# Optimization experiments

Hardware: AMD Instinct MI355X
Metric: run time of the kernel (lower is better)

## Reference

```python
import jax, jax.numpy as jnp
import numpy as np

SEQ, BATCH, D = 256, 4096, 100  # D = 2*hidden_size
STD = 0.05


def setup_inputs() -> dict:
    key = jax.random.key(0)
    k1, k2, k3, k4, k5 = jax.random.split(key, 5)
    return {
        "f_output": jax.random.normal(k1, (SEQ, BATCH, D), dtype=jnp.float32),
        "h_output": jax.random.normal(k2, (2, BATCH, D // 2), dtype=jnp.float32),
        "sentence_weight": jax.random.normal(k3, (D, D), dtype=jnp.float32) * STD,
        "sentence_bias": jax.random.normal(k4, (1, D), dtype=jnp.float32) * STD,
        "context_weight": jax.random.normal(k5, (D, 1), dtype=jnp.float32) * STD,
    }


def reference(f_output, h_output, sentence_weight, sentence_bias, context_weight):
    # matrix_mul: per-timestep mm + bias + tanh, vectorized over seq. [S,B,D]
    u = jnp.tanh(jnp.einsum('sbd,de->sbe', f_output, sentence_weight) + sentence_bias)
    # context projection (matrix_mul with no bias still applies tanh), squeeze -> [S,B]
    scores = jnp.tanh(jnp.einsum('sbd,dk->sbk', u, context_weight))[..., 0]
    # F.softmax on [B,S] defaults to dim=1 => softmax over seq
    attn = jax.nn.softmax(scores, axis=0)  # [S,B]
    # element_wise_mul: weighted sum over seq, keepdim -> [1,B,D]
    pooled = jnp.sum(f_output * attn[:, :, None], axis=0, keepdims=True)
    return (pooled, h_output)
```

## Files before the change

### kernel.cpp

```cpp
#include <hip/hip_runtime.h>
#include <hip/hip_bf16.h>

#define SEQ 256
#define BATCH 4096
#define DD 100
#define SB (BATCH * DD)
#define NBCOL 8
#define SCH 8
#define NCHUNK (SEQ / SCH)
#define ROWS (SCH * NBCOL)
#define SLAB_B (NBCOL * DD * 4)
#define WROWS_B (16 * DD * 4)

typedef __attribute__((ext_vector_type(8))) short bf16x8;
typedef __attribute__((ext_vector_type(4))) float f32x4;
typedef __attribute__((ext_vector_type(4))) unsigned u32x4;

#define WAIT_VM7  asm volatile("s_waitcnt vmcnt(7)" ::: "memory")
#define WAIT_VM0  asm volatile("s_waitcnt vmcnt(0)" ::: "memory")
#define WAIT_LGKM asm volatile("s_waitcnt lgkmcnt(0)" ::: "memory")

__device__ __forceinline__ short f2bf(float x) {
    __hip_bfloat16 hv = __float2bfloat16(x);
    return *reinterpret_cast<short*>(&hv);
}
__device__ __forceinline__ float bf2f_lo(unsigned int u) {
    return __builtin_bit_cast(float, u << 16);
}
__device__ __forceinline__ float bf2f_hi(unsigned int u) {
    return __builtin_bit_cast(float, u & 0xffff0000u);
}
__device__ __forceinline__ float fast_tanh(float x) {
    float ax = fabsf(x);
    float e  = __expf(-2.0f * ax);
    float t  = (1.0f - e) * __builtin_amdgcn_rcpf(1.0f + e);
    return copysignf(t, x);
}
__device__ __forceinline__ float pade_tanh(float x) {
    const float x2  = x * x;
    const float num = x * (27.0f + x2);
    const float den = fmaf(9.0f, x2, 27.0f);
    const float t   = num * __builtin_amdgcn_rcpf(den);
    return fminf(1.0f, fmaxf(-1.0f, t));
}
__device__ __forceinline__ unsigned pack_bf2(float lo, float hi) {
    return __builtin_amdgcn_perm(__builtin_bit_cast(unsigned, hi),
                                 __builtin_bit_cast(unsigned, lo),
                                 0x07060302u);
}

__global__ void prep_wfrag(const float* __restrict__ W, uint4* __restrict__ wsf) {
    const int idx = blockIdx.x * 256 + threadIdx.x;
    if (idx >= 28 * 64) return;
    const int l  = idx & 63;
    const int ft = idx >> 6;
    const int t  = ft & 3;
    const int n  = ft >> 2;
    const int col   = 16 * n + (l & 15);
    const int kbase = 32 * t + 8 * (l >> 4);
    unsigned short v[8];
    #pragma unroll
    for (int e = 0; e < 8; ++e) {
        const int k = kbase + e;
        const float w = (col < DD && k < DD) ? W[k * DD + col] : 0.0f;
        v[e] = (unsigned short)f2bf(w);
    }
    uint4 u;
    u.x = (unsigned)v[0] | ((unsigned)v[1] << 16);
    u.y = (unsigned)v[2] | ((unsigned)v[3] << 16);
    u.z = (unsigned)v[4] | ((unsigned)v[5] << 16);
    u.w = (unsigned)v[6] | ((unsigned)v[7] << 16);
    wsf[ft * 64 + l] = u;
}

__device__ __forceinline__ void stage_rows(const float* __restrict__ f,
                                           int s0, int b0, float* lbase,
                                           int wid, int lane) {
    const int base = WROWS_B * wid;
    #pragma unroll
    for (int r = 0; r < 6; ++r) {
        const int L   = base + (r << 10) + (lane << 4);
        const int s   = L / SLAB_B;
        const int rem = L - s * SLAB_B;
        const float* gp = f + (size_t)(s0 + s) * SB + (size_t)b0 * DD + (rem >> 2);
        __builtin_amdgcn_global_load_lds(
            (const __attribute__((address_space(1))) void*)gp,
            (__attribute__((address_space(3))) void*)((char*)lbase + L),
            16, 0, 0);
    }
    {
        const int L   = base + 6144 + (lane << 2);
        const int s   = L / SLAB_B;
        const int rem = L - s * SLAB_B;
        const float* gp = f + (size_t)(s0 + s) * SB + (size_t)b0 * DD + (rem >> 2);
        __builtin_amdgcn_global_load_lds(
            (const __attribute__((address_space(1))) void*)gp,
            (__attribute__((address_space(3))) void*)((char*)lbase + L),
            4, 0, 0);
    }
}

__global__ __launch_bounds__(256, 2)
void fused_sent_attn(const float* __restrict__ f,
                     const uint4* __restrict__ wsf,
                     const float* __restrict__ bias,
                     const float* __restrict__ cw,
                     const float* __restrict__ h,
                     float* __restrict__ out)
{
    __shared__ __align__(16) float fs[3][ROWS * DD];
    __shared__ uint4 wlds3[7 * 16];

    const int tid  = threadIdx.x;
    const int lane = tid & 63;
    const int wid  = tid >> 6;
    const int lr   = lane & 15;
    const int g    = lane >> 4;
    const int b0   = blockIdx.x * NBCOL;

    if (tid < 7 * 16) wlds3[tid] = wsf[(4 * (tid >> 4) + 3) * 64 + (tid & 15)];

    float bias_r[7], cw_r[7];
    #pragma unroll
    for (int n = 0; n < 7; ++n) {
        const int c = 16 * n + lr;
        bias_r[n] = (c < DD) ? bias[c] : 0.0f;
        cw_r[n]   = (c < DD) ? cw[c]   : 0.0f;
    }
    {
        const size_t obase = (size_t)BATCH * DD;
        const size_t HB = (size_t)BATCH * 50;
        if (tid < 200) {
            const int half = tid / 100, rem = tid - 100 * half;
            const float4* hs = reinterpret_cast<const float4*>(h + half * HB + (size_t)b0 * 50);
            float4* od = reinterpret_cast<float4*>(out + obase + half * HB + (size_t)b0 * 50);
            od[rem] = hs[rem];
        }
    }
    bf16x8 wr[21];
    #pragma unroll
    for (int n = 0; n < 7; ++n)
        #pragma unroll
        for (int t = 0; t < 3; ++t)
            wr[3 * n + t] = *reinterpret_cast<const bf16x8*>(&wsf[(4 * n + t) * 64 + lane]);
    WAIT_VM0;

    stage_rows(f, 0,   b0, fs[0], wid, lane);
    stage_rows(f, SCH, b0, fs[1], wid, lane);
    WAIT_VM7;
    WAIT_LGKM;
    __builtin_amdgcn_s_barrier();
    __builtin_amdgcn_sched_barrier(0);

    float pacc[4][8] = {{0}};
    float dreg = 0.0f;

    int cur = 0;
    for (int jc = 0; jc < NCHUNK; ++jc) {
        const int nxt2 = (cur + 2 >= 3) ? cur - 1 : cur + 2;

        if (jc + 2 < NCHUNK)
            stage_rows(f, (jc + 2) * SCH, b0, fs[nxt2], wid, lane);

        const float* rp = &fs[cur][(16 * wid + lr) * DD];
        bf16x8 a[4];
        #pragma unroll
        for (int t = 0; t < 3; ++t) {
            const float4 u0 = *reinterpret_cast<const float4*>(rp + 32 * t + 8 * g);
            const float4 u1 = *reinterpret_cast<const float4*>(rp + 32 * t + 8 * g + 4);
            u32x4 pk = {pack_bf2(u0.x, u0.y), pack_bf2(u0.z, u0.w),
                        pack_bf2(u1.x, u1.y), pack_bf2(u1.z, u1.w)};
            a[t] = __builtin_bit_cast(bf16x8, pk);
        }
        {
            u32x4 pk = {0u, 0u, 0u, 0u};
            if (g == 0) {
                const float4 u0 = *reinterpret_cast<const float4*>(rp + 96);
                pk.x = pack_bf2(u0.x, u0.y);
                pk.y = pack_bf2(u0.z, u0.w);
            }
            a[3] = __builtin_bit_cast(bf16x8, pk);
        }

        float scp[4] = {0, 0, 0, 0};
        #pragma unroll
        for (int n = 0; n < 7; ++n) {
            bf16x8 b3 = {0, 0, 0, 0, 0, 0, 0, 0};
            if (g == 0) b3 = *reinterpret_cast<const bf16x8*>(&wlds3[16 * n + lr]);
            f32x4 acc = {bias_r[n], bias_r[n], bias_r[n], bias_r[n]};
            acc = __builtin_amdgcn_mfma_f32_16x16x32_bf16(a[0], wr[3 * n + 0], acc, 0, 0, 0);
            acc = __builtin_amdgcn_mfma_f32_16x16x32_bf16(a[1], wr[3 * n + 1], acc, 0, 0, 0);
            acc = __builtin_amdgcn_mfma_f32_16x16x32_bf16(a[2], wr[3 * n + 2], acc, 0, 0, 0);
            acc = __builtin_amdgcn_mfma_f32_16x16x32_bf16(a[3], b3,            acc, 0, 0, 0);
            #pragma unroll
            for (int r = 0; r < 4; ++r)
                scp[r] = fmaf(pade_tanh(acc[r]), cw_r[n], scp[r]);
        }
        #pragma unroll
        for (int r = 0; r < 4; ++r) {
            float v = scp[r];
            v += __shfl_xor(v, 1);
            v += __shfl_xor(v, 2);
            v += __shfl_xor(v, 4);
            v += __shfl_xor(v, 8);
            scp[r] = v;
        }
        {
            const int src = (lr >> 2) << 4;
            const float tt0 = __shfl(scp[0], src);
            const float tt1 = __shfl(scp[1], src);
            const float tt2 = __shfl(scp[2], src);
            const float tt3 = __shfl(scp[3], src);
            const float ta = (lr & 1) ? tt1 : tt0;
            const float tb = (lr & 1) ? tt3 : tt2;
            const float Srow = (lr & 2) ? tb : ta;
            const float w = __expf(fast_tanh(Srow));

            #pragma unroll
            for (int t = 0; t < 4; ++t) {
                const u32x4 u = __builtin_bit_cast(u32x4, a[t]);
                #pragma unroll
                for (int j = 0; j < 4; ++j) {
                    pacc[t][2 * j]     = fmaf(w, bf2f_lo(u[j]), pacc[t][2 * j]);
                    pacc[t][2 * j + 1] = fmaf(w, bf2f_hi(u[j]), pacc[t][2 * j + 1]);
                }
            }
            dreg += w;
        }

        if (jc + 2 < NCHUNK) { WAIT_VM7; } else { WAIT_VM0; }
        __builtin_amdgcn_sched_barrier(0);
        cur = (cur + 1 >= 3) ? 0 : cur + 1;
    }

    float pv[4][8];
    #pragma unroll
    for (int t = 0; t < 4; ++t)
        #pragma unroll
        for (int e = 0; e < 8; ++e)
            pv[t][e] = pacc[t][e] + __shfl_xor(pacc[t][e], 8);
    const float dv = dreg + __shfl_xor(dreg, 8);

    __syncthreads();

    float* pool_sc = &fs[0][0];
    float* den_sc  = &fs[1][0];
    if (lr < 8) {
        float* dst = pool_sc + (wid * 8 + lr) * 104;
        #pragma unroll
        for (int t = 0; t < 3; ++t) {
            const int d0 = 32 * t + 8 * g;
            const float4 v0 = {pv[t][0], pv[t][1], pv[t][2], pv[t][3]};
            const float4 v1 = {pv[t][4], pv[t][5], pv[t][6], pv[t][7]};
            *reinterpret_cast<float4*>(dst + d0)     = v0;
            *reinterpret_cast<float4*>(dst + d0 + 4) = v1;
        }
        if (g == 0) {
            const float4 v0 = {pv[3][0], pv[3][1], pv[3][2], pv[3][3]};
            *reinterpret_cast<float4*>(dst + 96) = v0;
            den_sc[wid * 8 + lr] = dv;
        }
    }
    __syncthreads();

    if (tid < 200) {
        const int pb = tid / 25, q4 = tid % 25;
        f32x4 acc = {0.0f, 0.0f, 0.0f, 0.0f};
        float den = 0.0f;
        #pragma unroll
        for (int w2 = 0; w2 < 4; ++w2) {
            const f32x4 v = *reinterpret_cast<const f32x4*>(
                pool_sc + (w2 * 8 + pb) * 104 + 4 * q4);
            acc.x += v.x; acc.y += v.y; acc.z += v.z; acc.w += v.w;
            den += den_sc[w2 * 8 + pb];
        }
        const float rd = 1.0f / den;
        float4 o;
        o.x = acc.x * rd; o.y = acc.y * rd; o.z = acc.z * rd; o.w = acc.w * rd;
        *reinterpret_cast<float4*>(&out[(size_t)(b0 + pb) * DD + 4 * q4]) = o;
    }
}

extern "C" void kernel_launch(void* const* d_in, const int* in_sizes, int n_in,
                              void* d_out, int out_size, void* d_ws, size_t ws_size,
                              hipStream_t stream) {
    const float* f    = (const float*)d_in[0];
    const float* h    = (const float*)d_in[1];
    const float* W    = (const float*)d_in[2];
    const float* bias = (const float*)d_in[3];
    const float* cw   = (const float*)d_in[4];
    float* out = (float*)d_out;

    uint4* wsf = (uint4*)d_ws;

    prep_wfrag<<<7, 256, 0, stream>>>(W, wsf);
    fused_sent_attn<<<BATCH / NBCOL, 256, 0, stream>>>(f, wsf, bias, cw, h, out);
}
```

Baseline: 96.84 us.

## Split sequence across two block groups with partial sums and a combine kernel

Each block now covers 16 batch columns and half of the sequence, so every wave stages one contiguous per-timestep plane instead of 8x8 mixed rows. Each block writes unnormalized numerators and denominators to workspace, and a new combine kernel adds the two halves and divides. The grid size stays the same while the staging addressing gets simpler and the cross-lane shuffle reduction goes away. In exchange it adds an extra kernel launch and a round trip of partial results through global memory. The softmax skips max subtraction, which is valid because tanh bounds the scores.

```diff
diff --git a/kernel.cpp b/kernel.cpp
--- a/kernel.cpp
+++ b/kernel.cpp
@@ -5,12 +5,15 @@
 #define BATCH 4096
 #define DD 100
 #define SB (BATCH * DD)
-#define NBCOL 8
-#define SCH 8
-#define NCHUNK (SEQ / SCH)
+#define NBCOL 16
+#define SCH 4
+#define NSGRP 2
+#define SHALF (SEQ / NSGRP)
+#define NCHUNK (SHALF / SCH)
+#define NCGRP (BATCH / NBCOL)
 #define ROWS (SCH * NBCOL)
-#define SLAB_B (NBCOL * DD * 4)
-#define WROWS_B (16 * DD * 4)
+#define PLANE_B (NBCOL * DD * 4)
+#define PSTRIDE 1664
 
 typedef __attribute__((ext_vector_type(8))) short bf16x8;
 typedef __attribute__((ext_vector_type(4))) float f32x4;
@@ -73,40 +76,36 @@
     wsf[ft * 64 + l] = u;
 }
 
-__device__ __forceinline__ void stage_rows(const float* __restrict__ f,
-                                           int s0, int b0, float* lbase,
-                                           int wid, int lane) {
-    const int base = WROWS_B * wid;
+__device__ __forceinline__ void stage_plane(const float* __restrict__ f,
+                                            int s, int b0, float* lbase,
+                                            int wid, int lane) {
+    const int base = PLANE_B * wid;
+    const char* gp0 = (const char*)(f + (size_t)s * SB + (size_t)b0 * DD);
     #pragma unroll
     for (int r = 0; r < 6; ++r) {
-        const int L   = base + (r << 10) + (lane << 4);
-        const int s   = L / SLAB_B;
-        const int rem = L - s * SLAB_B;
-        const float* gp = f + (size_t)(s0 + s) * SB + (size_t)b0 * DD + (rem >> 2);
+        const int off = (r << 10) + (lane << 4);
         __builtin_amdgcn_global_load_lds(
-            (const __attribute__((address_space(1))) void*)gp,
-            (__attribute__((address_space(3))) void*)((char*)lbase + L),
+            (const __attribute__((address_space(1))) void*)(gp0 + off),
+            (__attribute__((address_space(3))) void*)((char*)lbase + base + off),
             16, 0, 0);
     }
     {
-        const int L   = base + 6144 + (lane << 2);
-        const int s   = L / SLAB_B;
-        const int rem = L - s * SLAB_B;
-        const float* gp = f + (size_t)(s0 + s) * SB + (size_t)b0 * DD + (rem >> 2);
+        const int off = 6144 + (lane << 2);
         __builtin_amdgcn_global_load_lds(
-            (const __attribute__((address_space(1))) void*)gp,
-            (__attribute__((address_space(3))) void*)((char*)lbase + L),
+            (const __attribute__((address_space(1))) void*)(gp0 + off),
+            (__attribute__((address_space(3))) void*)((char*)lbase + base + off),
             4, 0, 0);
     }
 }
 
 __global__ __launch_bounds__(256, 2)
-void fused_sent_attn(const float* __restrict__ f,
-                     const uint4* __restrict__ wsf,
-                     const float* __restrict__ bias,
-                     const float* __restrict__ cw,
-                     const float* __restrict__ h,
-                     float* __restrict__ out)
+void part_attn(const float* __restrict__ f,
+               const uint4* __restrict__ wsf,
+               const float* __restrict__ bias,
+               const float* __restrict__ cw,
+               const float* __restrict__ h,
+               float* __restrict__ out,
+               float* __restrict__ part)
 {
     __shared__ __align__(16) float fs[3][ROWS * DD];
     __shared__ uint4 wlds3[7 * 16];
@@ -116,7 +115,11 @@
     const int wid  = tid >> 6;
     const int lr   = lane & 15;
     const int g    = lane >> 4;
-    const int b0   = blockIdx.x * NBCOL;
+    const int bid  = blockIdx.x;
+    const int sgrp = bid >> 8;
+    const int cgrp = bid & (NCGRP - 1);
+    const int b0   = cgrp * NBCOL;
+    const int s_base = sgrp * SHALF;
 
     if (tid < 7 * 16) wlds3[tid] = wsf[(4 * (tid >> 4) + 3) * 64 + (tid & 15)];
 
@@ -127,11 +130,11 @@
         bias_r[n] = (c < DD) ? bias[c] : 0.0f;
         cw_r[n]   = (c < DD) ? cw[c]   : 0.0f;
     }
-    {
+    if (sgrp == 0) {
         const size_t obase = (size_t)BATCH * DD;
         const size_t HB = (size_t)BATCH * 50;
-        if (tid < 200) {
-            const int half = tid / 100, rem = tid - 100 * half;
+        for (int i = tid; i < 400; i += 256) {
+            const int half = i / 200, rem = i - 200 * half;
             const float4* hs = reinterpret_cast<const float4*>(h + half * HB + (size_t)b0 * 50);
             float4* od = reinterpret_cast<float4*>(out + obase + half * HB + (size_t)b0 * 50);
             od[rem] = hs[rem];
@@ -145,8 +148,8 @@
             wr[3 * n + t] = *reinterpret_cast<const bf16x8*>(&wsf[(4 * n + t) * 64 + lane]);
     WAIT_VM0;
 
-    stage_rows(f, 0,   b0, fs[0], wid, lane);
-    stage_rows(f, SCH, b0, fs[1], wid, lane);
+    stage_plane(f, s_base + wid,       b0, fs[0], wid, lane);
+    stage_plane(f, s_base + SCH + wid, b0, fs[1], wid, lane);
     WAIT_VM7;
     WAIT_LGKM;
     __builtin_amdgcn_s_barrier();
@@ -160,7 +163,7 @@
         const int nxt2 = (cur + 2 >= 3) ? cur - 1 : cur + 2;
 
         if (jc + 2 < NCHUNK)
-            stage_rows(f, (jc + 2) * SCH, b0, fs[nxt2], wid, lane);
+            stage_plane(f, s_base + (jc + 2) * SCH + wid, b0, fs[nxt2], wid, lane);
 
         const float* rp = &fs[cur][(16 * wid + lr) * DD];
         bf16x8 a[4];
@@ -233,52 +236,57 @@
         cur = (cur + 1 >= 3) ? 0 : cur + 1;
     }
 
-    float pv[4][8];
-    #pragma unroll
-    for (int t = 0; t < 4; ++t)
-        #pragma unroll
-        for (int e = 0; e < 8; ++e)
-            pv[t][e] = pacc[t][e] + __shfl_xor(pacc[t][e], 8);
-    const float dv = dreg + __shfl_xor(dreg, 8);
-
     __syncthreads();
 
     float* pool_sc = &fs[0][0];
-    float* den_sc  = &fs[1][0];
-    if (lr < 8) {
-        float* dst = pool_sc + (wid * 8 + lr) * 104;
+    float* den_sc  = &fs[2][0];
+    {
+        float* dst = pool_sc + (wid * 16 + lr) * 104;
         #pragma unroll
         for (int t = 0; t < 3; ++t) {
             const int d0 = 32 * t + 8 * g;
-            const float4 v0 = {pv[t][0], pv[t][1], pv[t][2], pv[t][3]};
-            const float4 v1 = {pv[t][4], pv[t][5], pv[t][6], pv[t][7]};
+            const float4 v0 = {pacc[t][0], pacc[t][1], pacc[t][2], pacc[t][3]};
+            const float4 v1 = {pacc[t][4], pacc[t][5], pacc[t][6], pacc[t][7]};
             *reinterpret_cast<float4*>(dst + d0)     = v0;
             *reinterpret_cast<float4*>(dst + d0 + 4) = v1;
         }
         if (g == 0) {
-            const float4 v0 = {pv[3][0], pv[3][1], pv[3][2], pv[3][3]};
+            const float4 v0 = {pacc[3][0], pacc[3][1], pacc[3][2], pacc[3][3]};
             *reinterpret_cast<float4*>(dst + 96) = v0;
-            den_sc[wid * 8 + lr] = dv;
+            den_sc[wid * 16 + lr] = dreg;
         }
     }
     __syncthreads();
 
-    if (tid < 200) {
-        const int pb = tid / 25, q4 = tid % 25;
+    float* rec = part + (size_t)bid * PSTRIDE;
+    for (int i = tid; i < 400; i += 256) {
+        const int col = i / 25, q4 = i - 25 * col;
         f32x4 acc = {0.0f, 0.0f, 0.0f, 0.0f};
-        float den = 0.0f;
         #pragma unroll
         for (int w2 = 0; w2 < 4; ++w2) {
             const f32x4 v = *reinterpret_cast<const f32x4*>(
-                pool_sc + (w2 * 8 + pb) * 104 + 4 * q4);
+                pool_sc + (w2 * 16 + col) * 104 + 4 * q4);
             acc.x += v.x; acc.y += v.y; acc.z += v.z; acc.w += v.w;
-            den += den_sc[w2 * 8 + pb];
-        }
-        const float rd = 1.0f / den;
-        float4 o;
-        o.x = acc.x * rd; o.y = acc.y * rd; o.z = acc.z * rd; o.w = acc.w * rd;
-        *reinterpret_cast<float4*>(&out[(size_t)(b0 + pb) * DD + 4 * q4]) = o;
-    }
+        }
+        *reinterpret_cast<float4*>(rec + col * DD + 4 * q4) =
+            *reinterpret_cast<float4*>(&acc);
+    }
+    if (tid < NBCOL) {
+        rec[1600 + tid] = den_sc[tid] + den_sc[16 + tid]
+                        + den_sc[32 + tid] + den_sc[48 + tid];
+    }
+}
+
+__global__ void combine(const float* __restrict__ part, float* __restrict__ out) {
+    const int idx = blockIdx.x * 256 + threadIdx.x;
+    if (idx >= BATCH * DD) return;
+    const int b = idx / DD, d = idx - b * DD;
+    const int cgrp = b >> 4, cl = b & 15;
+    const float* p0 = part + (size_t)cgrp * PSTRIDE;
+    const float* p1 = part + (size_t)(NCGRP + cgrp) * PSTRIDE;
+    const float num = p0[cl * DD + d] + p1[cl * DD + d];
+    const float den = p0[1600 + cl] + p1[1600 + cl];
+    out[idx] = num / den;
 }
 
 extern "C" void kernel_launch(void* const* d_in, const int* in_sizes, int n_in,
@@ -291,8 +299,10 @@
     const float* cw   = (const float*)d_in[4];
     float* out = (float*)d_out;
 
-    uint4* wsf = (uint4*)d_ws;
+    uint4* wsf  = (uint4*)d_ws;
+    float* part = (float*)((char*)d_ws + 32768);
 
     prep_wfrag<<<7, 256, 0, stream>>>(W, wsf);
-    fused_sent_attn<<<BATCH / NBCOL, 256, 0, stream>>>(f, wsf, bias, cw, h, out);
-}
+    part_attn<<<NSGRP * NCGRP, 256, 0, stream>>>(f, wsf, bias, cw, h, out, part);
+    combine<<<(BATCH * DD + 255) / 256, 256, 0, stream>>>(part, out);
+}
```

Result: slower. 100.4 us (+3.7%).

## Split sequence across two block groups with partial sums and combine kernel

Applied to the files above, without the earlier changes.

Splits the sequence reduction into two halves handled by separate blocks, doubling the grid from 512 to 1024 blocks. Each block writes unnormalized partial pooled sums and softmax denominators to workspace, and a new combine kernel adds them and divides. LDS staging goes from triple to double buffering, with the prefetch moved after compute, so occupancy can rise to 3 blocks per CU. The cost is an extra kernel launch, partial-sum traffic through global memory, and shallower prefetch depth.

```diff
diff --git a/kernel.cpp b/kernel.cpp
--- a/kernel.cpp
+++ b/kernel.cpp
@@ -7,10 +7,14 @@
 #define SB (BATCH * DD)
 #define NBCOL 8
 #define SCH 8
-#define NCHUNK (SEQ / SCH)
+#define NSGRP 2
+#define SHALF (SEQ / NSGRP)
+#define NCHUNK (SHALF / SCH)
+#define NCGRP (BATCH / NBCOL)
 #define ROWS (SCH * NBCOL)
 #define SLAB_B (NBCOL * DD * 4)
 #define WROWS_B (16 * DD * 4)
+#define PSTRIDE 832
 
 typedef __attribute__((ext_vector_type(8))) short bf16x8;
 typedef __attribute__((ext_vector_type(4))) float f32x4;
@@ -100,15 +104,16 @@
     }
 }
 
-__global__ __launch_bounds__(256, 2)
-void fused_sent_attn(const float* __restrict__ f,
-                     const uint4* __restrict__ wsf,
-                     const float* __restrict__ bias,
-                     const float* __restrict__ cw,
-                     const float* __restrict__ h,
-                     float* __restrict__ out)
+__global__ __launch_bounds__(256, 3)
+void part_attn(const float* __restrict__ f,
+               const uint4* __restrict__ wsf,
+               const float* __restrict__ bias,
+               const float* __restrict__ cw,
+               const float* __restrict__ h,
+               float* __restrict__ out,
+               float* __restrict__ part)
 {
-    __shared__ __align__(16) float fs[3][ROWS * DD];
+    __shared__ __align__(16) float fs[2][ROWS * DD];
     __shared__ uint4 wlds3[7 * 16];
 
     const int tid  = threadIdx.x;
@@ -116,7 +121,11 @@
     const int wid  = tid >> 6;
     const int lr   = lane & 15;
     const int g    = lane >> 4;
-    const int b0   = blockIdx.x * NBCOL;
+    const int bid  = blockIdx.x;
+    const int sgrp = bid >> 9;
+    const int cgrp = bid & (NCGRP - 1);
+    const int b0   = cgrp * NBCOL;
+    const int s_base = sgrp * SHALF;
 
     if (tid < 7 * 16) wlds3[tid] = wsf[(4 * (tid >> 4) + 3) * 64 + (tid & 15)];
 
@@ -127,15 +136,13 @@
         bias_r[n] = (c < DD) ? bias[c] : 0.0f;
         cw_r[n]   = (c < DD) ? cw[c]   : 0.0f;
     }
-    {
+    if (sgrp == 0 && tid < 200) {
         const size_t obase = (size_t)BATCH * DD;
         const size_t HB = (size_t)BATCH * 50;
-        if (tid < 200) {
-            const int half = tid / 100, rem = tid - 100 * half;
-            const float4* hs = reinterpret_cast<const float4*>(h + half * HB + (size_t)b0 * 50);
-            float4* od = reinterpret_cast<float4*>(out + obase + half * HB + (size_t)b0 * 50);
-            od[rem] = hs[rem];
-        }
+        const int half = tid / 100, rem = tid - 100 * half;
+        const float4* hs = reinterpret_cast<const float4*>(h + half * HB + (size_t)b0 * 50);
+        float4* od = reinterpret_cast<float4*>(out + obase + half * HB + (size_t)b0 * 50);
+        od[rem] = hs[rem];
     }
     bf16x8 wr[21];
     #pragma unroll
@@ -145,8 +152,8 @@
             wr[3 * n + t] = *reinterpret_cast<const bf16x8*>(&wsf[(4 * n + t) * 64 + lane]);
     WAIT_VM0;
 
-    stage_rows(f, 0,   b0, fs[0], wid, lane);
-    stage_rows(f, SCH, b0, fs[1], wid, lane);
+    stage_rows(f, s_base,       b0, fs[0], wid, lane);
+    stage_rows(f, s_base + SCH, b0, fs[1], wid, lane);
     WAIT_VM7;
     WAIT_LGKM;
     __builtin_amdgcn_s_barrier();
@@ -157,11 +164,6 @@
 
     int cur = 0;
     for (int jc = 0; jc < NCHUNK; ++jc) {
-        const int nxt2 = (cur + 2 >= 3) ? cur - 1 : cur + 2;
-
-        if (jc + 2 < NCHUNK)
-            stage_rows(f, (jc + 2) * SCH, b0, fs[nxt2], wid, lane);
-
         const float* rp = &fs[cur][(16 * wid + lr) * DD];
         bf16x8 a[4];
         #pragma unroll
@@ -228,9 +230,14 @@
             dreg += w;
         }
 
+        WAIT_LGKM;
+        __builtin_amdgcn_sched_barrier(0);
+        if (jc + 2 < NCHUNK)
+            stage_rows(f, s_base + (jc + 2) * SCH, b0, fs[cur], wid, lane);
+
         if (jc + 2 < NCHUNK) { WAIT_VM7; } else { WAIT_VM0; }
         __builtin_amdgcn_sched_barrier(0);
-        cur = (cur + 1 >= 3) ? 0 : cur + 1;
+        cur ^= 1;
     }
 
     float pv[4][8];
@@ -263,22 +270,34 @@
     }
     __syncthreads();
 
+    float* rec = part + (size_t)bid * PSTRIDE;
     if (tid < 200) {
         const int pb = tid / 25, q4 = tid % 25;
         f32x4 acc = {0.0f, 0.0f, 0.0f, 0.0f};
-        float den = 0.0f;
         #pragma unroll
         for (int w2 = 0; w2 < 4; ++w2) {
             const f32x4 v = *reinterpret_cast<const f32x4*>(
                 pool_sc + (w2 * 8 + pb) * 104 + 4 * q4);
             acc.x += v.x; acc.y += v.y; acc.z += v.z; acc.w += v.w;
-            den += den_sc[w2 * 8 + pb];
-        }
-        const float rd = 1.0f / den;
-        float4 o;
-        o.x = acc.x * rd; o.y = acc.y * rd; o.z = acc.z * rd; o.w = acc.w * rd;
-        *reinterpret_cast<float4*>(&out[(size_t)(b0 + pb) * DD + 4 * q4]) = o;
-    }
+        }
+        *reinterpret_cast<float4*>(rec + pb * DD + 4 * q4) =
+            *reinterpret_cast<float4*>(&acc);
+    } else if (tid < 208) {
+        const int pb = tid - 200;
+        rec[800 + pb] = den_sc[pb] + den_sc[8 + pb] + den_sc[16 + pb] + den_sc[24 + pb];
+    }
+}
+
+__global__ void combine(const float* __restrict__ part, float* __restrict__ out) {
+    const int idx = blockIdx.x * 256 + threadIdx.x;
+    if (idx >= BATCH * DD) return;
+    const int b = idx / DD, d = idx - b * DD;
+    const int cgrp = b >> 3, cl = b & 7;
+    const float* p0 = part + (size_t)cgrp * PSTRIDE;
+    const float* p1 = part + (size_t)(NCGRP + cgrp) * PSTRIDE;
+    const float num = p0[cl * DD + d] + p1[cl * DD + d];
+    const float den = p0[800 + cl] + p1[800 + cl];
+    out[idx] = num / den;
 }
 
 extern "C" void kernel_launch(void* const* d_in, const int* in_sizes, int n_in,
@@ -291,8 +310,10 @@
     const float* cw   = (const float*)d_in[4];
     float* out = (float*)d_out;
 
-    uint4* wsf = (uint4*)d_ws;
+    uint4* wsf  = (uint4*)d_ws;
+    float* part = (float*)((char*)d_ws + 32768);
 
     prep_wfrag<<<7, 256, 0, stream>>>(W, wsf);
-    fused_sent_attn<<<BATCH / NBCOL, 256, 0, stream>>>(f, wsf, bias, cw, h, out);
-}
+    part_attn<<<NSGRP * NCGRP, 256, 0, stream>>>(f, wsf, bias, cw, h, out, part);
+    combine<<<(BATCH * DD + 255) / 256, 256, 0, stream>>>(part, out);
+}
```

After: 326.2 us. +236.8%, slower.
